# Kernel tuning notes

Measured on AMD Instinct MI355X. Metric: run time of the kernel, lower is better.

Reference implementation:

```python
import jax, jax.numpy as jnp
import numpy as np

N_NODES = 50000
N_EDGES = 800000
D_IN = 128
D_HID = 128
D_OUT = 64
N_CONV = 4  # num_layers=5 -> 4 GINConv layers
BN_EPS = 1e-5


def setup_inputs() -> dict:
    key = jax.random.key(0)
    ks = jax.random.split(key, 16)
    h = jax.random.normal(ks[0], (N_NODES, D_IN), dtype=jnp.float32)
    src = jax.random.randint(ks[1], (N_EDGES,), 0, N_NODES)
    dst = jax.random.randint(ks[2], (N_EDGES,), 0, N_NODES)
    s = 0.05
    return {
        "h": h, "src": src, "dst": dst,
        # MLP inside each GINConv: Linear(no bias) -> BN -> ReLU -> Linear(no bias)
        "W1": jax.random.normal(ks[3], (N_CONV, D_IN, D_HID), dtype=jnp.float32) * s,
        "W2": jax.random.normal(ks[4], (N_CONV, D_HID, D_HID), dtype=jnp.float32) * s,
        "bn1_g": jnp.ones((N_CONV, D_HID), jnp.float32),
        "bn1_b": jnp.zeros((N_CONV, D_HID), jnp.float32),
        # outer BatchNorm after each GINConv
        "bn2_g": jnp.ones((N_CONV, D_HID), jnp.float32),
        "bn2_b": jnp.zeros((N_CONV, D_HID), jnp.float32),
        # 5 linear_prediction heads (layer 0 acts on input features)
        "pred_W": jax.random.normal(ks[5], (N_CONV + 1, D_HID, D_OUT), dtype=jnp.float32) * s,
        "pred_b": jnp.zeros((N_CONV + 1, D_OUT), jnp.float32),
    }


def _batchnorm(x, gamma, beta):
    # training-mode BatchNorm1d: batch statistics over the node dimension
    m = jnp.mean(x, axis=0)
    v = jnp.var(x, axis=0)
    return (x - m) * jax.lax.rsqrt(v + BN_EPS) * gamma + beta


def reference(h, src, dst, W1, W2, bn1_g, bn1_b, bn2_g, bn2_b, pred_W, pred_b):
    hidden_rep = [h]
    for i in range(N_CONV):
        # GINConv, learn_eps=False (eps=0): (1+eps)*h + sum of neighbor features
        agg = jax.ops.segment_sum(h[src], dst, num_segments=N_NODES)
        z = h + agg
        # MLP: Linear -> BN -> ReLU -> Linear
        z = z @ W1[i]
        z = jax.nn.relu(_batchnorm(z, bn1_g[i], bn1_b[i]))
        z = z @ W2[i]
        # outer BN + ReLU
        h = jax.nn.relu(_batchnorm(z, bn2_g[i], bn2_b[i]))
        hidden_rep.append(h)
    # SumPooling over the single graph, per-layer prediction heads (dropout = identity at eval)
    score = jnp.zeros((D_OUT,), h.dtype)
    for i, hr in enumerate(hidden_rep):
        pooled = jnp.sum(hr, axis=0)  # [D]
        score = score + pooled @ pred_W[i] + pred_b[i]
    return score  # [D_OUT], matches .view(shape[1])
```

## Files before the change

### kernel.cpp

```cpp
#include <hip/hip_runtime.h>
#include <hip/hip_bf16.h>

#define N_NODES 50000
#define N_EDGES 800000
#define D 128

typedef __bf16 bf16;
typedef __attribute__((ext_vector_type(8))) __bf16 bf16x8;
typedef __attribute__((ext_vector_type(4))) __bf16 bf16x4;
typedef __attribute__((ext_vector_type(16))) float f32x16;
typedef _Float16 f16;
typedef __attribute__((ext_vector_type(2))) _Float16 f16x2;
typedef __attribute__((ext_vector_type(4))) _Float16 f16x4;
typedef __attribute__((ext_vector_type(8))) _Float16 f16x8;

__global__ __launch_bounds__(256)
void initprep_kernel(const float* __restrict__ W1, const float* __restrict__ W2,
                     bf16* __restrict__ WfH, bf16* __restrict__ WfL,
                     int* __restrict__ deg, float* __restrict__ stats,
                     float* __restrict__ ppart, float* __restrict__ plglob,
                     float* __restrict__ pooled4, int* __restrict__ done,
                     int* __restrict__ flags, const float* __restrict__ h0,
                     f16* __restrict__ Hb) {
    int b = blockIdx.x, t = threadIdx.x;
    if (b < 64) {
        int gid = b * 256 + t;
        int lane = gid & 63;
        int grp = gid >> 6;
        int sub = grp & 7;
        int cf = (grp >> 3) & 3;
        int m = grp >> 5;
        const float* Wsrc = (m < 4) ? (W1 + m * 16384) : (W2 + (m - 4) * 16384);
        int col = cf * 32 + (lane & 31);
        int kb = sub * 16 + 8 * (lane >> 5);
        bf16x8 h, l;
#pragma unroll
        for (int j = 0; j < 8; ++j) {
            float w = Wsrc[(kb + j) * 128 + col];
            bf16 hb = (bf16)w;
            bf16 lb = (bf16)(w - (float)hb);
            h[j] = hb;
            l[j] = lb;
        }
        int idx = m * 16384 + ((grp & 31) * 64 + lane) * 8;
        *(bf16x8*)&WfH[idx] = h;
        *(bf16x8*)&WfL[idx] = l;
    } else if (b < 260) {
        int i = (b - 64) * 256 + t;
        if (i < N_NODES) deg[i] = 0;
        if (i < 2048) stats[i] = 0.f;
        if (i < 32768) ppart[i] = 0.f;
        if (i < 512) plglob[i] = 0.f;
        if (i < 128) pooled4[i] = 0.f;
        if (i < 2) done[i] = 0;
        if (i < 196) flags[i] = 0;
    } else {
        int c = (t & 31) << 2;
        int rrow = t >> 5;
        for (int r = (b - 260) * 8 + rrow; r < N_NODES; r += 512 * 8) {
            float4 v = *(const float4*)&h0[r * D + c];
            f16x4 h4;
            h4[0] = (f16)v.x; h4[1] = (f16)v.y; h4[2] = (f16)v.z; h4[3] = (f16)v.w;
            *(f16x4*)&Hb[r * D + c] = h4;
        }
    }
}

__global__ void hist_kernel(const int* __restrict__ dst, int* __restrict__ deg) {
    int e = blockIdx.x * 256 + threadIdx.x;
    atomicAdd(&deg[dst[e]], 1);
}

__global__ __launch_bounds__(256)
void scan_kernel(const int* __restrict__ deg, int* __restrict__ bsum,
                 int* __restrict__ flags, int* __restrict__ row_start,
                 int* __restrict__ cursor) {
    __shared__ int s[256];
    __shared__ int rsum[256];
    int t = threadIdx.x, b = blockIdx.x;
    int g = b * 256 + t;
    int v = (g < N_NODES) ? deg[g] : 0;
    s[t] = v;
    __syncthreads();
    for (int off = 1; off < 256; off <<= 1) {
        int a = (t >= off) ? s[t - off] : 0;
        __syncthreads();
        s[t] += a;
        __syncthreads();
    }
    if (t == 0) {
        __hip_atomic_store(&bsum[b], s[255], __ATOMIC_RELEASE, __HIP_MEMORY_SCOPE_AGENT);
        __hip_atomic_store(&flags[b], 1, __ATOMIC_RELEASE, __HIP_MEMORY_SCOPE_AGENT);
    }
    int part = 0;
    for (int j = t; j < b; j += 256) {
        while (__hip_atomic_load(&flags[j], __ATOMIC_ACQUIRE, __HIP_MEMORY_SCOPE_AGENT) == 0) {}
        part += __hip_atomic_load(&bsum[j], __ATOMIC_ACQUIRE, __HIP_MEMORY_SCOPE_AGENT);
    }
    rsum[t] = part;
    __syncthreads();
    for (int off = 128; off > 0; off >>= 1) {
        if (t < off) rsum[t] += rsum[t + off];
        __syncthreads();
    }
    int excl = rsum[0] + s[t] - v;
    if (g < N_NODES) {
        row_start[g] = excl;
        cursor[g] = excl;
    }
    if (b == 0 && t == 0) row_start[N_NODES] = N_EDGES;
}

__global__ void fill_kernel(const int* __restrict__ src, const int* __restrict__ dst,
                            int* __restrict__ cursor, int* __restrict__ esrc) {
    int e = blockIdx.x * 256 + threadIdx.x;
    int d = dst[e];
    int p = atomicAdd(&cursor[d], 1);
    esrc[p] = src[e];
}

template <bool APPLY>
__global__ __launch_bounds__(256)
void agg_kernel(const f16* __restrict__ H, const int* __restrict__ esrc,
                const int* __restrict__ row_start, const float* __restrict__ stats,
                const float* __restrict__ gam, const float* __restrict__ bet,
                f16* __restrict__ Z, float* __restrict__ ppart) {
    __shared__ float sred[4][128];
    int wv = threadIdx.x >> 6;
    int v = blockIdx.x * 4 + wv;
    int lane = threadIdx.x & 63;
    int c2 = lane << 1;
    float a0 = 1.f, b0 = 0.f, a1 = 1.f, b1 = 0.f;
    if (APPLY) {
        float m0 = stats[c2] * (1.0f / N_NODES);
        float q0 = stats[128 + c2] * (1.0f / N_NODES);
        float g0 = gam[c2] * rsqrtf(q0 - m0 * m0 + 1e-5f);
        a0 = g0; b0 = bet[c2] - m0 * g0;
        float m1 = stats[c2 + 1] * (1.0f / N_NODES);
        float q1 = stats[128 + c2 + 1] * (1.0f / N_NODES);
        float g1 = gam[c2 + 1] * rsqrtf(q1 - m1 * m1 + 1e-5f);
        a1 = g1; b1 = bet[c2 + 1] - m1 * g1;
    }
    int beg = row_start[v], end_ = row_start[v + 1];
    f16x2 sv = *(const f16x2*)&H[v * D + c2];
    float ax = (float)sv[0], ay = (float)sv[1];
    if (APPLY) {
        ax = fmaxf(fmaf(a0, ax, b0), 0.f);
        ay = fmaxf(fmaf(a1, ay, b1), 0.f);
    }
    sred[wv][c2] = ax;
    sred[wv][c2 + 1] = ay;
    int e = beg;
    for (; e + 4 <= end_; e += 4) {
        int s0 = esrc[e], s1 = esrc[e + 1], s2 = esrc[e + 2], s3 = esrc[e + 3];
        f16x2 v0 = *(const f16x2*)&H[s0 * D + c2];
        f16x2 v1 = *(const f16x2*)&H[s1 * D + c2];
        f16x2 v2 = *(const f16x2*)&H[s2 * D + c2];
        f16x2 v3 = *(const f16x2*)&H[s3 * D + c2];
        if (APPLY) {
            ax += fmaxf(fmaf(a0, (float)v0[0], b0), 0.f) + fmaxf(fmaf(a0, (float)v1[0], b0), 0.f)
                + fmaxf(fmaf(a0, (float)v2[0], b0), 0.f) + fmaxf(fmaf(a0, (float)v3[0], b0), 0.f);
            ay += fmaxf(fmaf(a1, (float)v0[1], b1), 0.f) + fmaxf(fmaf(a1, (float)v1[1], b1), 0.f)
                + fmaxf(fmaf(a1, (float)v2[1], b1), 0.f) + fmaxf(fmaf(a1, (float)v3[1], b1), 0.f);
        } else {
            ax += (float)v0[0] + (float)v1[0] + (float)v2[0] + (float)v3[0];
            ay += (float)v0[1] + (float)v1[1] + (float)v2[1] + (float)v3[1];
        }
    }
    for (; e < end_; ++e) {
        int s0 = esrc[e];
        f16x2 v0 = *(const f16x2*)&H[s0 * D + c2];
        if (APPLY) {
            ax += fmaxf(fmaf(a0, (float)v0[0], b0), 0.f);
            ay += fmaxf(fmaf(a1, (float)v0[1], b1), 0.f);
        } else {
            ax += (float)v0[0];
            ay += (float)v0[1];
        }
    }
    f16x2 zv;
    zv[0] = (f16)ax;
    zv[1] = (f16)ay;
    *(f16x2*)&Z[v * D + c2] = zv;
    __syncthreads();
    int t = threadIdx.x;
    if (t < 128) {
        float s = sred[0][t] + sred[1][t] + sred[2][t] + sred[3][t];
        atomicAdd(&ppart[(blockIdx.x & 63) * 128 + t], s);
    }
}

template <bool BN_IN>
__global__ __launch_bounds__(256, 2)
void mm_kernel(const f16* __restrict__ X, const bf16* __restrict__ WfH,
               const bf16* __restrict__ WfL, const float* __restrict__ stats_in,
               const float* __restrict__ gam, const float* __restrict__ bet,
               f16* __restrict__ Y, float* __restrict__ stats_out) {
    __shared__ bf16 Ah[4096];
    __shared__ bf16 Al[4096];
    __shared__ float ab[2][128];

    int t = threadIdx.x;
    int w = t >> 6, lane = t & 63;
    if (BN_IN && t < 128) {
        float s = stats_in[t] * (1.0f / N_NODES);
        float q = stats_in[128 + t] * (1.0f / N_NODES);
        float a = gam[t] * rsqrtf(q - s * s + 1e-5f);
        ab[0][t] = a;
        ab[1][t] = bet[t] - s * a;
    }

    bf16x8 Bh[8], Bl[8];
#pragma unroll
    for (int c = 0; c < 8; ++c) {
        int idx = ((w * 8 + c) * 64 + lane) * 8;
        Bh[c] = *(const bf16x8*)&WfH[idx];
        Bl[c] = *(const bf16x8*)&WfL[idx];
    }

    f32x16 acc[4];
#pragma unroll
    for (int fr = 0; fr < 4; ++fr) acc[fr] = (f32x16)0.0f;

    int rowbase = blockIdx.x * 128;
    int nrows = min(128, N_NODES - rowbase);
    int srow = t >> 1;
    int sk0 = (t & 1) * 16;
    __syncthreads();

    for (int kb = 0; kb < 4; ++kb) {
        if (kb) __syncthreads();
        {
            float vf[16];
#pragma unroll
            for (int j = 0; j < 16; ++j) vf[j] = 0.f;
            if (srow < nrows) {
                const f16* xr = &X[(rowbase + srow) * D + kb * 32 + sk0];
                f16x8 u0 = *(const f16x8*)&xr[0];
                f16x8 u1 = *(const f16x8*)&xr[8];
#pragma unroll
                for (int j = 0; j < 8; ++j) {
                    vf[j] = (float)u0[j];
                    vf[8 + j] = (float)u1[j];
                }
                if (BN_IN) {
#pragma unroll
                    for (int j = 0; j < 16; ++j) {
                        int kg = kb * 32 + sk0 + j;
                        vf[j] = fmaxf(fmaf(ab[0][kg], vf[j], ab[1][kg]), 0.f);
                    }
                }
            }
#pragma unroll
            for (int i = 0; i < 4; ++i) {
                bf16x4 h4, l4;
#pragma unroll
                for (int j = 0; j < 4; ++j) {
                    bf16 hb = (bf16)vf[i * 4 + j];
                    h4[j] = hb;
                    l4[j] = (bf16)(vf[i * 4 + j] - (float)hb);
                }
                int e = srow * 32 + sk0 + i * 4;
                int es = e ^ ((srow & 7) << 3);
                *(bf16x4*)&Ah[es] = h4;
                *(bf16x4*)&Al[es] = l4;
            }
        }
        __syncthreads();
#pragma unroll
        for (int s2 = 0; s2 < 2; ++s2) {
            int sg = kb * 2 + s2;
#pragma unroll
            for (int fr = 0; fr < 4; ++fr) {
                int row = fr * 32 + (lane & 31);
                int e = row * 32 + s2 * 16 + 8 * (lane >> 5);
                int es = e ^ ((row & 7) << 3);
                bf16x8 ah = *(const bf16x8*)&Ah[es];
                bf16x8 al = *(const bf16x8*)&Al[es];
                acc[fr] = __builtin_amdgcn_mfma_f32_32x32x16_bf16(al, Bh[sg], acc[fr], 0, 0, 0);
                acc[fr] = __builtin_amdgcn_mfma_f32_32x32x16_bf16(ah, Bl[sg], acc[fr], 0, 0, 0);
                acc[fr] = __builtin_amdgcn_mfma_f32_32x32x16_bf16(ah, Bh[sg], acc[fr], 0, 0, 0);
            }
        }
    }

    int col = w * 32 + (lane & 31);
    float psum = 0.f, psq = 0.f;
#pragma unroll
    for (int fr = 0; fr < 4; ++fr) {
#pragma unroll
        for (int r = 0; r < 16; ++r) {
            float v = acc[fr][r];
            int row = fr * 32 + (r & 3) + 8 * (r >> 2) + 4 * (lane >> 5);
            if (row < nrows) Y[(rowbase + row) * D + col] = (f16)v;
            psum += v;
            psq += v * v;
        }
    }
    psum += __shfl_xor(psum, 32);
    psq += __shfl_xor(psq, 32);
    if (lane < 32) {
        atomicAdd(&stats_out[col], psum);
        atomicAdd(&stats_out[128 + col], psq);
    }
}

__global__ __launch_bounds__(256)
void pool4head_kernel(const f16* __restrict__ Y, const float* __restrict__ stats,
                      const float* __restrict__ gam, const float* __restrict__ bet,
                      const float* __restrict__ ppart, float* __restrict__ plglob,
                      float* __restrict__ pooled4, const float* __restrict__ pW,
                      const float* __restrict__ pB, float* __restrict__ out,
                      int* __restrict__ done) {
    __shared__ float abS[2][128];
    __shared__ float red[8][128];
    __shared__ int lastflag;
    int t = threadIdx.x, b = blockIdx.x;

    if (b < 4 && t < 128) {
        float s = 0.f;
#pragma unroll
        for (int sl = 0; sl < 64; ++sl) s += ppart[b * 8192 + sl * 128 + t];
        __hip_atomic_store(&plglob[b * 128 + t], s, __ATOMIC_RELEASE,
                           __HIP_MEMORY_SCOPE_AGENT);
    }

    if (t < 128) {
        float s = stats[t] * (1.0f / N_NODES);
        float q = stats[128 + t] * (1.0f / N_NODES);
        float a = gam[t] * rsqrtf(q - s * s + 1e-5f);
        abS[0][t] = a;
        abS[1][t] = bet[t] - s * a;
    }
    __syncthreads();
    int c = (t & 31) << 2;
    int rrow = t >> 5;
    float4 A = *(const float4*)&abS[0][c];
    float4 B = *(const float4*)&abS[1][c];
    float4 p = make_float4(0.f, 0.f, 0.f, 0.f);
    for (int r = b * 8 + rrow; r < N_NODES; r += gridDim.x * 8) {
        f16x4 v = *(const f16x4*)&Y[r * D + c];
        p.x += fmaxf(fmaf(A.x, (float)v[0], B.x), 0.f);
        p.y += fmaxf(fmaf(A.y, (float)v[1], B.y), 0.f);
        p.z += fmaxf(fmaf(A.z, (float)v[2], B.z), 0.f);
        p.w += fmaxf(fmaf(A.w, (float)v[3], B.w), 0.f);
    }
    *(float4*)&red[rrow][c] = p;
    __syncthreads();
    if (t < 128) {
        float s = 0.f;
#pragma unroll
        for (int i = 0; i < 8; ++i) s += red[i][t];
        atomicAdd(&pooled4[t], s);
    }
    __syncthreads();
    if (t == 0) {
        __threadfence();
        int v = atomicAdd(&done[1], 1);
        lastflag = (v == (int)gridDim.x - 1);
    }
    __syncthreads();
    if (!lastflag) return;

    __shared__ float pl[5][128];
    __shared__ float red2[4][64];
    if (t < 128) {
#pragma unroll
        for (int l = 0; l < 4; ++l)
            pl[l][t] = __hip_atomic_load(&plglob[l * 128 + t], __ATOMIC_ACQUIRE,
                                         __HIP_MEMORY_SCOPE_AGENT);
        pl[4][t] = __hip_atomic_load(&pooled4[t], __ATOMIC_ACQUIRE,
                                     __HIP_MEMORY_SCOPE_AGENT);
    }
    __syncthreads();
    int o = t & 63, q = t >> 6;
    float acc0 = 0.f, acc1 = 0.f;
#pragma unroll
    for (int l = 0; l < 5; ++l) {
        const float* wp = pW + l * 8192;
#pragma unroll
        for (int cc = 0; cc < 16; ++cc) {
            int c0 = q * 32 + cc;
            int c1 = q * 32 + 16 + cc;
            acc0 += pl[l][c0] * wp[c0 * 64 + o];
            acc1 += pl[l][c1] * wp[c1 * 64 + o];
        }
    }
    red2[q][o] = acc0 + acc1;
    __syncthreads();
    if (t < 64) {
        float s = red2[0][t] + red2[1][t] + red2[2][t] + red2[3][t];
#pragma unroll
        for (int l = 0; l < 5; ++l) s += pB[l * 64 + t];
        out[t] = s;
    }
}

extern "C" void kernel_launch(void* const* d_in, const int* in_sizes, int n_in,
                              void* d_out, int out_size, void* d_ws, size_t ws_size,
                              hipStream_t stream) {
    const float* h0 = (const float*)d_in[0];
    const int* src = (const int*)d_in[1];
    const int* dst = (const int*)d_in[2];
    const float* W1 = (const float*)d_in[3];
    const float* W2 = (const float*)d_in[4];
    const float* bn1_g = (const float*)d_in[5];
    const float* bn1_b = (const float*)d_in[6];
    const float* bn2_g = (const float*)d_in[7];
    const float* bn2_b = (const float*)d_in[8];
    const float* pW = (const float*)d_in[9];
    const float* pB = (const float*)d_in[10];
    float* out = (float*)d_out;

    char* ws = (char*)d_ws;
    f16* B0 = (f16*)(ws + 0);
    f16* B1 = (f16*)(ws + 12800000);
    f16* B2 = (f16*)(ws + 25600000);
    int* esrc = (int*)(ws + 38400000);
    int* deg = (int*)(ws + 41600000);
    int* row_start = (int*)(ws + 41800000);
    int* cursor = (int*)(ws + 42000016);
    int* bsum = (int*)(ws + 42200016);
    int* flags = (int*)(ws + 42200800);
    int* done = (int*)(ws + 42201600);
    float* stats = (float*)(ws + 42201664);
    float* ppart = (float*)(ws + 42209856);
    float* plglob = (float*)(ws + 42340928);
    float* pooled4 = (float*)(ws + 42342976);
    bf16* WfH = (bf16*)(ws + 42343488);
    bf16* WfL = (bf16*)(ws + 42605632);

    initprep_kernel<<<772, 256, 0, stream>>>(W1, W2, WfH, WfL, deg, stats, ppart, plglob,
                                             pooled4, done, flags, h0, B0);
    hist_kernel<<<3125, 256, 0, stream>>>(dst, deg);
    scan_kernel<<<196, 256, 0, stream>>>(deg, bsum, flags, row_start, cursor);
    fill_kernel<<<3125, 256, 0, stream>>>(src, dst, cursor, esrc);

    for (int i = 0; i < 4; ++i) {
        if (i == 0) {
            agg_kernel<false><<<12500, 256, 0, stream>>>(B0, esrc, row_start, nullptr,
                                                         nullptr, nullptr, B1, ppart);
        } else {
            agg_kernel<true><<<12500, 256, 0, stream>>>(
                B0, esrc, row_start, stats + (4 + i - 1) * 256, bn2_g + (i - 1) * 128,
                bn2_b + (i - 1) * 128, B1, ppart + i * 8192);
        }
        mm_kernel<false><<<391, 256, 0, stream>>>(B1, WfH + i * 16384, WfL + i * 16384,
                                                  nullptr, nullptr, nullptr, B2,
                                                  stats + i * 256);
        mm_kernel<true><<<391, 256, 0, stream>>>(B2, WfH + (4 + i) * 16384,
                                                 WfL + (4 + i) * 16384, stats + i * 256,
                                                 bn1_g + i * 128, bn1_b + i * 128, B0,
                                                 stats + (4 + i) * 256);
    }
    pool4head_kernel<<<512, 256, 0, stream>>>(B0, stats + 7 * 256, bn2_g + 3 * 128,
                                              bn2_b + 3 * 128, ppart, plglob, pooled4, pW,
                                              pB, out, done);
}
```

Measured before the change: 542.8 us.

## Build CSR via two-pass bucketed sort instead of global histogram/scan/fill

Replaces the global-atomic histogram, decoupled-lookback scan and atomic fill with a two-pass bucket sort. The first pass bins edges into 98 coarse dst buckets of 512 nodes each, using shared-memory counts. The second pass builds per-bucket local prefix sums and scatters src ids with shared-memory atomics. This removes 1.6M global atomics and one kernel launch. The cost is an extra 6.4MB intermediate buffer, and the fixed bucket capacity (16384) could overflow on skewed degree distributions.

```diff
diff --git a/kernel.cpp b/kernel.cpp
--- a/kernel.cpp
+++ b/kernel.cpp
@@ -4,6 +4,8 @@
 #define N_NODES 50000
 #define N_EDGES 800000
 #define D 128
+#define NBUCK 98
+#define BCAP 16384
 
 typedef __bf16 bf16;
 typedef __attribute__((ext_vector_type(8))) __bf16 bf16x8;
@@ -17,11 +19,10 @@
 __global__ __launch_bounds__(256)
 void initprep_kernel(const float* __restrict__ W1, const float* __restrict__ W2,
                      bf16* __restrict__ WfH, bf16* __restrict__ WfL,
-                     int* __restrict__ deg, float* __restrict__ stats,
+                     int* __restrict__ bucketCnt, float* __restrict__ stats,
                      float* __restrict__ ppart, float* __restrict__ plglob,
                      float* __restrict__ pooled4, int* __restrict__ done,
-                     int* __restrict__ flags, const float* __restrict__ h0,
-                     f16* __restrict__ Hb) {
+                     const float* __restrict__ h0, f16* __restrict__ Hb) {
     int b = blockIdx.x, t = threadIdx.x;
     if (b < 64) {
         int gid = b * 256 + t;
@@ -47,13 +48,12 @@
         *(bf16x8*)&WfL[idx] = l;
     } else if (b < 260) {
         int i = (b - 64) * 256 + t;
-        if (i < N_NODES) deg[i] = 0;
+        if (i < NBUCK) bucketCnt[i] = 0;
         if (i < 2048) stats[i] = 0.f;
         if (i < 32768) ppart[i] = 0.f;
         if (i < 512) plglob[i] = 0.f;
         if (i < 128) pooled4[i] = 0.f;
         if (i < 2) done[i] = 0;
-        if (i < 196) flags[i] = 0;
     } else {
         int c = (t & 31) << 2;
         int rrow = t >> 5;
@@ -66,57 +66,77 @@
     }
 }
 
-__global__ void hist_kernel(const int* __restrict__ dst, int* __restrict__ deg) {
-    int e = blockIdx.x * 256 + threadIdx.x;
-    atomicAdd(&deg[dst[e]], 1);
-}
-
 __global__ __launch_bounds__(256)
-void scan_kernel(const int* __restrict__ deg, int* __restrict__ bsum,
-                 int* __restrict__ flags, int* __restrict__ row_start,
-                 int* __restrict__ cursor) {
-    __shared__ int s[256];
-    __shared__ int rsum[256];
-    int t = threadIdx.x, b = blockIdx.x;
-    int g = b * 256 + t;
-    int v = (g < N_NODES) ? deg[g] : 0;
-    s[t] = v;
+void bucket1_kernel(const int* __restrict__ src, const int* __restrict__ dst,
+                    int* __restrict__ bucketCnt, int2* __restrict__ bstore) {
+    __shared__ int2 ed[6250];
+    __shared__ int cnt[NBUCK];
+    __shared__ int offs[NBUCK];
+    __shared__ int lcur[NBUCK];
+    int b = blockIdx.x, t = threadIdx.x;
+    int e0 = b * 6250;
+    for (int i = t; i < 6250; i += 256) ed[i] = make_int2(src[e0 + i], dst[e0 + i]);
+    if (t < NBUCK) { cnt[t] = 0; lcur[t] = 0; }
+    __syncthreads();
+    for (int i = t; i < 6250; i += 256) atomicAdd(&cnt[ed[i].y >> 9], 1);
+    __syncthreads();
+    if (t < NBUCK) offs[t] = atomicAdd(&bucketCnt[t], cnt[t]);
+    __syncthreads();
+    for (int i = t; i < 6250; i += 256) {
+        int2 e = ed[i];
+        int k = e.y >> 9;
+        int li = atomicAdd(&lcur[k], 1);
+        bstore[k * BCAP + offs[k] + li] = e;
+    }
+}
+
+__global__ __launch_bounds__(256)
+void bucket2_kernel(const int* __restrict__ bucketCnt, const int2* __restrict__ bstore,
+                    int* __restrict__ row_start, int* __restrict__ esrc) {
+    __shared__ int ps[256];
+    __shared__ int cnt[512];
+    __shared__ int cur[512];
+    int k = blockIdx.x, t = threadIdx.x;
+    ps[t] = (t < NBUCK) ? bucketCnt[t] : 0;
     __syncthreads();
     for (int off = 1; off < 256; off <<= 1) {
-        int a = (t >= off) ? s[t - off] : 0;
+        int a = (t >= off) ? ps[t - off] : 0;
         __syncthreads();
-        s[t] += a;
+        ps[t] += a;
         __syncthreads();
     }
-    if (t == 0) {
-        __hip_atomic_store(&bsum[b], s[255], __ATOMIC_RELEASE, __HIP_MEMORY_SCOPE_AGENT);
-        __hip_atomic_store(&flags[b], 1, __ATOMIC_RELEASE, __HIP_MEMORY_SCOPE_AGENT);
-    }
-    int part = 0;
-    for (int j = t; j < b; j += 256) {
-        while (__hip_atomic_load(&flags[j], __ATOMIC_ACQUIRE, __HIP_MEMORY_SCOPE_AGENT) == 0) {}
-        part += __hip_atomic_load(&bsum[j], __ATOMIC_ACQUIRE, __HIP_MEMORY_SCOPE_AGENT);
-    }
-    rsum[t] = part;
-    __syncthreads();
-    for (int off = 128; off > 0; off >>= 1) {
-        if (t < off) rsum[t] += rsum[t + off];
+    int base = (k == 0) ? 0 : ps[k - 1];
+    int n = bucketCnt[k];
+    cnt[t] = 0;
+    cnt[t + 256] = 0;
+    __syncthreads();
+    const int2* bp = &bstore[k * BCAP];
+    for (int i = t; i < n; i += 256) atomicAdd(&cnt[bp[i].y & 511], 1);
+    __syncthreads();
+    int x0 = cnt[2 * t], x1 = cnt[2 * t + 1];
+    ps[t] = x0 + x1;
+    __syncthreads();
+    for (int off = 1; off < 256; off <<= 1) {
+        int a = (t >= off) ? ps[t - off] : 0;
         __syncthreads();
-    }
-    int excl = rsum[0] + s[t] - v;
-    if (g < N_NODES) {
-        row_start[g] = excl;
-        cursor[g] = excl;
-    }
-    if (b == 0 && t == 0) row_start[N_NODES] = N_EDGES;
-}
-
-__global__ void fill_kernel(const int* __restrict__ src, const int* __restrict__ dst,
-                            int* __restrict__ cursor, int* __restrict__ esrc) {
-    int e = blockIdx.x * 256 + threadIdx.x;
-    int d = dst[e];
-    int p = atomicAdd(&cursor[d], 1);
-    esrc[p] = src[e];
+        ps[t] += a;
+        __syncthreads();
+    }
+    int ep = (t == 0) ? 0 : ps[t - 1];
+    int c0 = base + ep;
+    int c1 = base + ep + x0;
+    cur[2 * t] = c0;
+    cur[2 * t + 1] = c1;
+    int g0 = (k << 9) + 2 * t;
+    if (g0 < N_NODES) row_start[g0] = c0;
+    if (g0 + 1 < N_NODES) row_start[g0 + 1] = c1;
+    if (k == NBUCK - 1 && t == 0) row_start[N_NODES] = N_EDGES;
+    __syncthreads();
+    for (int i = t; i < n; i += 256) {
+        int2 e = bp[i];
+        int p = atomicAdd(&cur[e.y & 511], 1);
+        esrc[p] = e.x;
+    }
 }
 
 template <bool APPLY>
@@ -417,24 +437,21 @@
     f16* B1 = (f16*)(ws + 12800000);
     f16* B2 = (f16*)(ws + 25600000);
     int* esrc = (int*)(ws + 38400000);
-    int* deg = (int*)(ws + 41600000);
-    int* row_start = (int*)(ws + 41800000);
-    int* cursor = (int*)(ws + 42000016);
-    int* bsum = (int*)(ws + 42200016);
-    int* flags = (int*)(ws + 42200800);
-    int* done = (int*)(ws + 42201600);
-    float* stats = (float*)(ws + 42201664);
-    float* ppart = (float*)(ws + 42209856);
-    float* plglob = (float*)(ws + 42340928);
-    float* pooled4 = (float*)(ws + 42342976);
-    bf16* WfH = (bf16*)(ws + 42343488);
-    bf16* WfL = (bf16*)(ws + 42605632);
-
-    initprep_kernel<<<772, 256, 0, stream>>>(W1, W2, WfH, WfL, deg, stats, ppart, plglob,
-                                             pooled4, done, flags, h0, B0);
-    hist_kernel<<<3125, 256, 0, stream>>>(dst, deg);
-    scan_kernel<<<196, 256, 0, stream>>>(deg, bsum, flags, row_start, cursor);
-    fill_kernel<<<3125, 256, 0, stream>>>(src, dst, cursor, esrc);
+    int2* bstore = (int2*)(ws + 41600016);
+    int* bucketCnt = (int*)(ws + 54445072);
+    int* row_start = (int*)(ws + 54445472);
+    int* done = (int*)(ws + 54645504);
+    float* stats = (float*)(ws + 54645568);
+    float* ppart = (float*)(ws + 54653760);
+    float* plglob = (float*)(ws + 54784832);
+    float* pooled4 = (float*)(ws + 54786880);
+    bf16* WfH = (bf16*)(ws + 54787392);
+    bf16* WfL = (bf16*)(ws + 55049536);
+
+    initprep_kernel<<<772, 256, 0, stream>>>(W1, W2, WfH, WfL, bucketCnt, stats, ppart,
+                                             plglob, pooled4, done, h0, B0);
+    bucket1_kernel<<<128, 256, 0, stream>>>(src, dst, bucketCnt, bstore);
+    bucket2_kernel<<<NBUCK, 256, 0, stream>>>(bucketCnt, bstore, row_start, esrc);
 
     for (int i = 0; i < 4; ++i) {
         if (i == 0) {
```

Result: faster. 475.8 us (-12.3%).
